# Kernel optimization log

Hardware: AMD Instinct MI355X
Metric: run time of the kernel (lower is better)

The kernel has to match this reference:

```python
import jax, jax.numpy as jnp
import numpy as np

N = 8192
D = 256
LN_EPS = 1e-5
NORM_EPS = 1e-12


def _layernorm(h, gamma, beta):
    mu = jnp.mean(h, axis=-1, keepdims=True)
    var = jnp.var(h, axis=-1, keepdims=True)
    return (h - mu) * jax.lax.rsqrt(var + LN_EPS) * gamma + beta


def _elu(z):
    return jnp.where(z > 0, z, jnp.expm1(z))


def setup_inputs() -> dict:
    key = jax.random.key(0)
    ks = jax.random.split(key, 5)
    s = 1.0 / np.sqrt(D)  # torch Linear default-ish init scale
    h = jax.random.normal(ks[0], (N, D), dtype=jnp.float32)
    x = jax.random.normal(ks[1], (N, D), dtype=jnp.float32)
    Wk = jax.random.normal(ks[2], (D, D), dtype=jnp.float32) * s
    Wq = jax.random.normal(ks[3], (D, D), dtype=jnp.float32) * s
    Wv = jax.random.normal(ks[4], (D, D), dtype=jnp.float32) * s
    ln_gamma = jnp.ones((D,), dtype=jnp.float32)
    ln_beta = jnp.zeros((D,), dtype=jnp.float32)
    semantic_weight = -1.0
    mixing = jnp.array([[semantic_weight, semantic_weight], [0.0, 0.0]], dtype=jnp.float32)
    return {"h": h, "x": x, "Wk": Wk, "Wq": Wq, "Wv": Wv,
            "ln_gamma": ln_gamma, "ln_beta": ln_beta, "mixing": mixing}


def reference(h, x, Wk, Wq, Wv, ln_gamma, ln_beta, mixing):
    h0, x0 = h, x
    hn = _layernorm(h, ln_gamma, ln_beta)                      # [N, D]
    k = hn @ Wk                                                # [N, H]
    q = hn @ Wq                                                # [N, H]
    # semantic attention: softmax over rows of k q^T / sqrt(H)
    a_h = jax.nn.softmax((k @ q.T) * (D ** -0.5), axis=-1)     # [N, N]
    # structural attention: row-L2-normalized gram matrix of x
    g = x @ x.T                                                # [N, N]
    gnorm = jnp.linalg.norm(g, axis=-1, keepdims=True)
    a_x = g / jnp.maximum(gnorm, NORM_EPS)
    # learned 2x2 mixing, softmax over dim 0 (stack @ mixing.softmax(0))
    m = jax.nn.softmax(mixing, axis=0)
    a_h_mix = a_h * m[0, 0] + a_x * m[1, 0]
    a_x_mix = a_h * m[0, 1] + a_x * m[1, 1]
    h_new = _elu((a_h_mix @ hn) @ Wv)                          # [N, D]
    x_new = a_x_mix @ x                                        # [N, D]
    h_new = h_new + h0
    x_new = x_new + x0
    return (h_new, x_new)
```

## Files before the change

kernel.cpp:

```cpp
#include <hip/hip_runtime.h>

#define N 8192
#define D 256

typedef unsigned short u16;
typedef unsigned int u32;
typedef short bf16x8 __attribute__((ext_vector_type(8)));
typedef float f32x4 __attribute__((ext_vector_type(4)));

__device__ __forceinline__ u16 f2bf(float f) {
    u32 u = __float_as_uint(f);
    u += 0x7FFFu + ((u >> 16) & 1u);
    return (u16)(u >> 16);
}
__device__ __forceinline__ float bf2f(u16 v) {
    return __uint_as_float(((u32)v) << 16);
}

#define MFMA(a, b, c) __builtin_amdgcn_mfma_f32_16x16x32_bf16((a), (b), (c), 0, 0, 0)

__global__ __launch_bounds__(256) void k_prep_ln(const float* __restrict__ h,
    const float* __restrict__ x, const float* __restrict__ gamma,
    const float* __restrict__ beta, u16* __restrict__ hnb, u16* __restrict__ xb)
{
    int lane = threadIdx.x & 63;
    int row = blockIdx.x * 4 + (threadIdx.x >> 6);
    const float4 hv = ((const float4*)(h + (size_t)row * D))[lane];
    float s = hv.x + hv.y + hv.z + hv.w;
    float s2 = hv.x * hv.x + hv.y * hv.y + hv.z * hv.z + hv.w * hv.w;
#pragma unroll
    for (int m = 1; m < 64; m <<= 1) { s += __shfl_xor(s, m); s2 += __shfl_xor(s2, m); }
    float mu = s * (1.0f / D);
    float var = s2 * (1.0f / D) - mu * mu;
    float rstd = rsqrtf(var + 1e-5f);
    const float4 gv = ((const float4*)gamma)[lane];
    const float4 bv = ((const float4*)beta)[lane];
    ushort4 o;
    o.x = f2bf((hv.x - mu) * rstd * gv.x + bv.x);
    o.y = f2bf((hv.y - mu) * rstd * gv.y + bv.y);
    o.z = f2bf((hv.z - mu) * rstd * gv.z + bv.z);
    o.w = f2bf((hv.w - mu) * rstd * gv.w + bv.w);
    ((ushort4*)(hnb + (size_t)row * D))[lane] = o;
    const float4 xv = ((const float4*)(x + (size_t)row * D))[lane];
    ushort4 xo;
    xo.x = f2bf(xv.x); xo.y = f2bf(xv.y); xo.z = f2bf(xv.z); xo.w = f2bf(xv.w);
    ((ushort4*)(xb + (size_t)row * D))[lane] = xo;
}

__global__ void k_wT(const float* __restrict__ Wk, const float* __restrict__ Wq,
                     const float* __restrict__ Wv, u16* __restrict__ wkT,
                     u16* __restrict__ wqT, u16* __restrict__ wvT)
{
    const float* src = blockIdx.y == 0 ? Wk : (blockIdx.y == 1 ? Wq : Wv);
    u16* dst = blockIdx.y == 0 ? wkT : (blockIdx.y == 1 ? wqT : wvT);
    int c = blockIdx.x, r = threadIdx.x;
    dst[c * D + r] = f2bf(src[r * D + c]);
}

__global__ __launch_bounds__(256) void k_transpose(const u16* __restrict__ s0,
    u16* __restrict__ d0, const u16* __restrict__ s1, u16* __restrict__ d1)
{
    const u16* src = blockIdx.y ? s1 : s0;
    u16* dst = blockIdx.y ? d1 : d0;
    int jb = (blockIdx.x & 127) * 64;
    int cb = (blockIdx.x >> 7) * 64;
    __shared__ u16 tile[64][72];
    int t = threadIdx.x;
#pragma unroll
    for (int i = 0; i < 2; ++i) {
        int id = t + i * 256;
        int r = id >> 3, ch = id & 7;
        uint4 v = *(const uint4*)(src + (size_t)(jb + r) * D + cb + ch * 8);
        *(uint4*)(&tile[r][ch * 8]) = v;
    }
    __syncthreads();
#pragma unroll
    for (int i = 0; i < 2; ++i) {
        int id = t + i * 256;
        int c = id >> 3, rch = id & 7;
        u16 vals[8] __attribute__((aligned(16)));
#pragma unroll
        for (int e = 0; e < 8; ++e) vals[e] = tile[rch * 8 + e][c];
        *(uint4*)(dst + (size_t)(cb + c) * N + jb + rch * 8) = *(const uint4*)vals;
    }
}

__global__ __launch_bounds__(256, 4) void k_proj_kq(const u16* __restrict__ A,
    const u16* __restrict__ wkT, const u16* __restrict__ wqT,
    u16* __restrict__ kb, u16* __restrict__ qb)
{
    int w = threadIdx.x >> 6;
    int lane = threadIdx.x & 63;
    int l16 = lane & 15, lhi = lane >> 4;
    int rows = blockIdx.x * 16;
    const u16* BT = (w >> 1) ? wqT : wkT;
    u16* out = (w >> 1) ? qb : kb;
    int colbase = (w & 1) * 128;
    const f32x4 z4 = {0.f, 0.f, 0.f, 0.f};
    f32x4 acc[8] = {z4, z4, z4, z4, z4, z4, z4, z4};
#pragma unroll
    for (int ks = 0; ks < 8; ++ks) {
        bf16x8 a = *(const bf16x8*)(A + (size_t)(rows + l16) * D + ks * 32 + lhi * 8);
#pragma unroll
        for (int cf = 0; cf < 8; ++cf) {
            bf16x8 b = *(const bf16x8*)(BT + (size_t)(colbase + cf * 16 + l16) * D + ks * 32 + lhi * 8);
            acc[cf] = MFMA(a, b, acc[cf]);
        }
    }
#pragma unroll
    for (int cf = 0; cf < 8; ++cf)
#pragma unroll
        for (int jj = 0; jj < 4; ++jj)
            out[(size_t)(rows + lhi * 4 + jj) * D + colbase + cf * 16 + l16] = f2bf(acc[cf][jj]);
}

__global__ __launch_bounds__(256) void k_small_nt(const u16* __restrict__ hnT,
    const u16* __restrict__ xT, float* __restrict__ part)
{
    const u16* P = blockIdx.y ? hnT : xT;
    const u16* Q = xT;
    int w = threadIdx.x >> 6;
    int lane = threadIdx.x & 63;
    int l16 = lane & 15, lhi = lane >> 4;
    int arow = blockIdx.x * 16;
    int bcol = w * 64;
    int n0b = blockIdx.z * 1024;
    const f32x4 z4 = {0.f, 0.f, 0.f, 0.f};
    f32x4 acc[4] = {z4, z4, z4, z4};
    for (int n0 = n0b; n0 < n0b + 1024; n0 += 32) {
        bf16x8 a = *(const bf16x8*)(P + (size_t)(arow + l16) * N + n0 + lhi * 8);
#pragma unroll
        for (int cf = 0; cf < 4; ++cf) {
            bf16x8 b = *(const bf16x8*)(Q + (size_t)(bcol + cf * 16 + l16) * N + n0 + lhi * 8);
            acc[cf] = MFMA(a, b, acc[cf]);
        }
    }
    float* dst = part + ((size_t)blockIdx.z * 2 + blockIdx.y) * 65536;
#pragma unroll
    for (int cf = 0; cf < 4; ++cf)
#pragma unroll
        for (int jj = 0; jj < 4; ++jj)
            dst[(size_t)(arow + lhi * 4 + jj) * D + bcol + cf * 16 + l16] = acc[cf][jj];
}

__global__ __launch_bounds__(256) void k_cast(const float* __restrict__ part,
    u16* __restrict__ Mb, u16* __restrict__ XHT)
{
    int t = blockIdx.x * 256 + threadIdx.x;
    int side = t >> 16, idx = t & 65535;
    float s = 0.f;
#pragma unroll
    for (int ks = 0; ks < 8; ++ks) s += part[((size_t)ks * 2 + side) * 65536 + idx];
    (side ? XHT : Mb)[idx] = f2bf(s);
}

template <int EPI>
__global__ __launch_bounds__(256, 4) void k_gemm16(const u16* __restrict__ A,
    const u16* __restrict__ BT, u16* __restrict__ outb,
    const float* __restrict__ res, float* __restrict__ outf)
{
    int w = threadIdx.x >> 6;
    int lane = threadIdx.x & 63;
    int l16 = lane & 15, lhi = lane >> 4;
    int rows = blockIdx.x * 16;
    int cols = w * 64;
    const f32x4 z4 = {0.f, 0.f, 0.f, 0.f};
    f32x4 acc[4] = {z4, z4, z4, z4};
#pragma unroll
    for (int ks = 0; ks < 8; ++ks) {
        bf16x8 a = *(const bf16x8*)(A + (size_t)(rows + l16) * D + ks * 32 + lhi * 8);
#pragma unroll
        for (int cf = 0; cf < 4; ++cf) {
            bf16x8 b = *(const bf16x8*)(BT + (size_t)(cols + cf * 16 + l16) * D + ks * 32 + lhi * 8);
            acc[cf] = MFMA(a, b, acc[cf]);
        }
    }
#pragma unroll
    for (int cf = 0; cf < 4; ++cf)
#pragma unroll
        for (int jj = 0; jj < 4; ++jj) {
            int r = rows + lhi * 4 + jj;
            int c = cols + cf * 16 + l16;
            float v = acc[cf][jj];
            if (EPI == 0) {
                outb[(size_t)r * D + c] = f2bf(v);
            } else {
                float z = v > 0.f ? v : expm1f(v);
                outf[(size_t)r * D + c] = z + res[(size_t)r * D + c];
            }
        }
}

__global__ __launch_bounds__(512, 4) void k_fused(const u16* __restrict__ kb,
    const u16* __restrict__ qb, const u16* __restrict__ hnT,
    const u16* __restrict__ xT, u16* __restrict__ accP, float* __restrict__ lpart)
{
    __shared__ u16 AK[64 * 256];
    __shared__ u16 P[64 * 256];
    const int tid = threadIdx.x;
    const int w = tid >> 6;
    const int lane = tid & 63;
    const int l16 = lane & 15, lhi = lane >> 4;
    const int wgid = blockIdx.x;
    const int xcd = wgid & 7;
    const int js = xcd >> 1;
    const int rb = ((wgid >> 3) << 1) | (xcd & 1);
    const int R0 = rb * 64;
    const int jbase = js * 2048;

    {
        int r = tid >> 3, sb = (tid & 7) * 4;
        const u16* src = kb + (size_t)(R0 + r) * D + sb * 8;
#pragma unroll
        for (int i = 0; i < 4; ++i) {
            bf16x8 v = *(const bf16x8*)(src + i * 8);
            int slotp = ((sb + i) + 4 * r) & 31;
            *(bf16x8*)(AK + r * 256 + slotp * 8) = v;
        }
    }
    __syncthreads();

    const int rg = w & 1;
    const int jf = w >> 1;
    const int t2 = w >> 2;
    const int ch = w & 3;
    const u16* T = t2 ? xT : hnT;
    const u16* Tb0 = T + (size_t)(ch * 64 + 0 * 16 + l16) * N + lhi * 8;
    const u16* Tb1 = T + (size_t)(ch * 64 + 1 * 16 + l16) * N + lhi * 8;
    const u16* Tb2 = T + (size_t)(ch * 64 + 2 * 16 + l16) * N + lhi * 8;
    const u16* Tb3 = T + (size_t)(ch * 64 + 3 * 16 + l16) * N + lhi * 8;

    const f32x4 z4 = {0.f, 0.f, 0.f, 0.f};
    f32x4 acc[16];
#pragma unroll
    for (int i = 0; i < 16; ++i) acc[i] = z4;
    f32x4 red2[2] = {z4, z4};
    bf16x8 tp0[4], tp1[4];

    for (int it = 0; it < 8; ++it) {
        const int jb = jbase + it * 256;
        asm volatile("s_waitcnt lgkmcnt(0)\n\ts_barrier" ::: "memory");

#pragma unroll
        for (int s = 0; s < 2; ++s) {
            const int jc = jb + s * 128 + jf * 32;
            f32x4 cs00 = z4, cs01 = z4, cs10 = z4, cs11 = z4;
#pragma unroll
            for (int ks = 0; ks < 8; ++ks) {
                int r0 = rg * 32 + l16;
                int r1 = rg * 32 + 16 + l16;
                int sl0 = ((ks * 4 + lhi) + 4 * r0) & 31;
                int sl1 = ((ks * 4 + lhi) + 4 * r1) & 31;
                bf16x8 a0 = *(const bf16x8*)(AK + r0 * 256 + sl0 * 8);
                bf16x8 a1 = *(const bf16x8*)(AK + r1 * 256 + sl1 * 8);
                const u16* Bq = qb + (size_t)(jc + l16) * D + ks * 32 + lhi * 8;
                bf16x8 b0 = *(const bf16x8*)(Bq);
                bf16x8 b1 = *(const bf16x8*)(Bq + 16 * D);
                cs00 = MFMA(a0, b0, cs00);
                cs01 = MFMA(a0, b1, cs01);
                cs10 = MFMA(a1, b0, cs10);
                cs11 = MFMA(a1, b1, cs11);
            }
#pragma unroll
            for (int rf = 0; rf < 2; ++rf)
#pragma unroll
                for (int cfr = 0; cfr < 2; ++cfr) {
                    f32x4 s4 = rf ? (cfr ? cs11 : cs10) : (cfr ? cs01 : cs00);
#pragma unroll
                    for (int jj = 0; jj < 4; ++jj) {
                        int row = rg * 32 + rf * 16 + lhi * 4 + jj;
                        int col = s * 128 + jf * 32 + cfr * 16 + l16;
                        float pv = __expf(s4[jj] * 0.0625f);
                        red2[rf][jj] += pv;
                        int slot = (col >> 3) ^ (row & 15);
                        *(u16*)((char*)P + row * 512 + slot * 16 + (col & 7) * 2) = f2bf(pv);
                    }
                }
        }
        tp0[0] = *(const bf16x8*)(Tb0 + jb); tp0[1] = *(const bf16x8*)(Tb1 + jb);
        tp0[2] = *(const bf16x8*)(Tb2 + jb); tp0[3] = *(const bf16x8*)(Tb3 + jb);
        tp1[0] = *(const bf16x8*)(Tb0 + jb + 32); tp1[1] = *(const bf16x8*)(Tb1 + jb + 32);
        tp1[2] = *(const bf16x8*)(Tb2 + jb + 32); tp1[3] = *(const bf16x8*)(Tb3 + jb + 32);
        asm volatile("s_waitcnt lgkmcnt(0)\n\ts_barrier" ::: "memory");

        __builtin_amdgcn_s_setprio(1);
        const char* Pb = (const char*)P;
#define PV_STEP(KF, TP)                                                             \
        {                                                                           \
            bf16x8 pa0 = *(const bf16x8*)(Pb + (0 * 16 + l16) * 512 + ((((KF) * 4 + lhi) ^ l16) << 4)); \
            bf16x8 pa1 = *(const bf16x8*)(Pb + (1 * 16 + l16) * 512 + ((((KF) * 4 + lhi) ^ l16) << 4)); \
            bf16x8 pa2 = *(const bf16x8*)(Pb + (2 * 16 + l16) * 512 + ((((KF) * 4 + lhi) ^ l16) << 4)); \
            bf16x8 pa3 = *(const bf16x8*)(Pb + (3 * 16 + l16) * 512 + ((((KF) * 4 + lhi) ^ l16) << 4)); \
            acc[0]  = MFMA(pa0, TP[0], acc[0]);  acc[1]  = MFMA(pa0, TP[1], acc[1]);  \
            acc[2]  = MFMA(pa0, TP[2], acc[2]);  acc[3]  = MFMA(pa0, TP[3], acc[3]);  \
            acc[4]  = MFMA(pa1, TP[0], acc[4]);  acc[5]  = MFMA(pa1, TP[1], acc[5]);  \
            acc[6]  = MFMA(pa1, TP[2], acc[6]);  acc[7]  = MFMA(pa1, TP[3], acc[7]);  \
            acc[8]  = MFMA(pa2, TP[0], acc[8]);  acc[9]  = MFMA(pa2, TP[1], acc[9]);  \
            acc[10] = MFMA(pa2, TP[2], acc[10]); acc[11] = MFMA(pa2, TP[3], acc[11]); \
            acc[12] = MFMA(pa3, TP[0], acc[12]); acc[13] = MFMA(pa3, TP[1], acc[13]); \
            acc[14] = MFMA(pa3, TP[2], acc[14]); acc[15] = MFMA(pa3, TP[3], acc[15]); \
            if ((KF) + 2 < 8) {                                                     \
                TP[0] = *(const bf16x8*)(Tb0 + jb + ((KF) + 2) * 32);               \
                TP[1] = *(const bf16x8*)(Tb1 + jb + ((KF) + 2) * 32);               \
                TP[2] = *(const bf16x8*)(Tb2 + jb + ((KF) + 2) * 32);               \
                TP[3] = *(const bf16x8*)(Tb3 + jb + ((KF) + 2) * 32);               \
            }                                                                       \
        }
        PV_STEP(0, tp0)
        PV_STEP(1, tp1)
        PV_STEP(2, tp0)
        PV_STEP(3, tp1)
        PV_STEP(4, tp0)
        PV_STEP(5, tp1)
        PV_STEP(6, tp0)
        PV_STEP(7, tp1)
#undef PV_STEP
        __builtin_amdgcn_s_setprio(0);
    }

    {
        u16* base = accP + ((((size_t)js * 128 + rb) * 8 + w) * 64) * 64 + lane;
#pragma unroll
        for (int rf = 0; rf < 4; ++rf)
#pragma unroll
            for (int cf = 0; cf < 4; ++cf)
#pragma unroll
                for (int jj = 0; jj < 4; ++jj) {
                    int v = (rf * 4 + cf) * 4 + jj;
                    __builtin_nontemporal_store(f2bf(acc[rf * 4 + cf][jj]), base + (size_t)v * 64);
                }
    }
#pragma unroll
    for (int rf = 0; rf < 2; ++rf)
#pragma unroll
        for (int m = 1; m < 16; m <<= 1) {
            red2[rf][0] += __shfl_xor(red2[rf][0], m);
            red2[rf][1] += __shfl_xor(red2[rf][1], m);
            red2[rf][2] += __shfl_xor(red2[rf][2], m);
            red2[rf][3] += __shfl_xor(red2[rf][3], m);
        }
    if (l16 == 0)
#pragma unroll
        for (int rf = 0; rf < 2; ++rf)
#pragma unroll
            for (int jj = 0; jj < 4; ++jj)
                atomicAdd(lpart + R0 + rg * 32 + rf * 16 + lhi * 4 + jj, red2[rf][jj]);
}

__global__ __launch_bounds__(256) void k_stats(const float* __restrict__ lpart,
    const u16* __restrict__ Ux, const u16* __restrict__ xb,
    const float* __restrict__ mixing, float* __restrict__ stats)
{
    int lane = threadIdx.x & 63;
    int row = blockIdx.x * 4 + (threadIdx.x >> 6);
    float sg = 0.f;
    {
        ushort4 yv = ((const ushort4*)(Ux + (size_t)row * D))[lane];
        ushort4 xv = ((const ushort4*)(xb + (size_t)row * D))[lane];
        sg += bf2f(yv.x) * bf2f(xv.x);
        sg += bf2f(yv.y) * bf2f(xv.y);
        sg += bf2f(yv.z) * bf2f(xv.z);
        sg += bf2f(yv.w) * bf2f(xv.w);
    }
#pragma unroll
    for (int m = 1; m < 64; m <<= 1) sg += __shfl_xor(sg, m);
    if (lane == 0) {
        float inv_l = 1.0f / lpart[row];
        float inv_g = 1.0f / fmaxf(sqrtf(fmaxf(sg, 0.f)), 1e-12f);
        float e00 = __expf(mixing[0]), e10 = __expf(mixing[2]);
        float c00 = e00 / (e00 + e10), c10 = e10 / (e00 + e10);
        float e01 = __expf(mixing[1]), e11 = __expf(mixing[3]);
        float c01 = e01 / (e01 + e11), c11 = e11 / (e01 + e11);
        float4 stv = { c00 * inv_l, c10 * inv_g, c01 * inv_l, c11 * inv_g };
        ((float4*)stats)[row] = stv;
    }
}

__global__ __launch_bounds__(256) void k_combine(const u16* __restrict__ accP,
    const float* __restrict__ stats, const u16* __restrict__ Uh,
    const u16* __restrict__ Ux, const float* __restrict__ x0,
    u16* __restrict__ hmixb, float* __restrict__ outx)
{
    int t = blockIdx.x * 256 + threadIdx.x;
    int r = t >> 7;
    int q = t & 127;
    int rb = r >> 6, rr = r & 63;
    int t2 = q >> 6;
    int cc = (q & 63) * 4;
    int wv = t2 * 4 + (cc >> 6);
    int rf = rr >> 4, lhi = (rr >> 2) & 3, jj = rr & 3;
    int cf = (cc >> 4) & 3, l16 = cc & 15;
    int v = (rf * 4 + cf) * 4 + jj;
    int lane = lhi * 16 + l16;
    float v0 = 0.f, v1 = 0.f, v2 = 0.f, v3 = 0.f;
#pragma unroll
    for (int s = 0; s < 4; ++s) {
        const u16* bp = accP + ((((size_t)s * 128 + rb) * 8 + wv) * 64 + v) * 64 + lane;
        ushort4 a = *(const ushort4*)bp;
        v0 += bf2f(a.x); v1 += bf2f(a.y); v2 += bf2f(a.z); v3 += bf2f(a.w);
    }
    float4 st = ((const float4*)stats)[r];
    if (t2 == 0) {
        int c = cc;
        ushort4 u = *(const ushort4*)(Uh + (size_t)r * D + c);
        ushort4 o;
        o.x = f2bf(st.x * v0 + st.y * bf2f(u.x));
        o.y = f2bf(st.x * v1 + st.y * bf2f(u.y));
        o.z = f2bf(st.x * v2 + st.y * bf2f(u.z));
        o.w = f2bf(st.x * v3 + st.y * bf2f(u.w));
        *(ushort4*)(hmixb + (size_t)r * D + c) = o;
    } else {
        int c = cc;
        ushort4 u = *(const ushort4*)(Ux + (size_t)r * D + c);
        float4 xv = *(const float4*)(x0 + (size_t)r * D + c);
        float4 o;
        o.x = st.z * v0 + st.w * bf2f(u.x) + xv.x;
        o.y = st.z * v1 + st.w * bf2f(u.y) + xv.y;
        o.z = st.z * v2 + st.w * bf2f(u.z) + xv.z;
        o.w = st.z * v3 + st.w * bf2f(u.w) + xv.w;
        *(float4*)(outx + (size_t)r * D + c) = o;
    }
}

extern "C" void kernel_launch(void* const* d_in, const int* in_sizes, int n_in,
                              void* d_out, int out_size, void* d_ws, size_t ws_size,
                              hipStream_t stream)
{
    const float* h = (const float*)d_in[0];
    const float* x = (const float*)d_in[1];
    const float* Wk = (const float*)d_in[2];
    const float* Wq = (const float*)d_in[3];
    const float* Wv = (const float*)d_in[4];
    const float* gamma = (const float*)d_in[5];
    const float* beta = (const float*)d_in[6];
    const float* mixing = (const float*)d_in[7];

    char* p = (char*)d_ws;
    const size_t ND2 = (size_t)N * D * 2;
    u16* hnb = (u16*)p; p += ND2;
    u16* xb = (u16*)p; p += ND2;
    u16* kb = (u16*)p; p += ND2;
    u16* qb = (u16*)p; p += ND2;
    u16* hnT = (u16*)p; p += ND2;
    u16* xT = (u16*)p; p += ND2;
    u16* Ux = (u16*)p; p += ND2;
    u16* wkT = (u16*)p; p += (size_t)D * D * 2;
    u16* wqT = (u16*)p; p += (size_t)D * D * 2;
    u16* wvT = (u16*)p; p += (size_t)D * D * 2;
    u16* Mb = (u16*)p; p += (size_t)D * D * 2;
    u16* XHT = (u16*)p; p += (size_t)D * D * 2;
    u16* accP = (u16*)p; p += (size_t)4 * N * 512 * 2;
    float* ntpart = (float*)accP;
    float* lpart = (float*)p; p += (size_t)N * 4;
    float* stats = (float*)p; p += (size_t)N * 4 * 4;
    u16* Uh = hnb;
    u16* hmixb = kb;

    float* outh = (float*)d_out;
    float* outx = outh + (size_t)N * D;

    hipMemsetAsync(lpart, 0, (size_t)N * 4, stream);
    k_prep_ln<<<N / 4, 256, 0, stream>>>(h, x, gamma, beta, hnb, xb);
    k_wT<<<dim3(256, 3), 256, 0, stream>>>(Wk, Wq, Wv, wkT, wqT, wvT);
    k_transpose<<<dim3(512, 2), 256, 0, stream>>>(hnb, hnT, xb, xT);
    k_proj_kq<<<512, 256, 0, stream>>>(hnb, wkT, wqT, kb, qb);
    k_small_nt<<<dim3(16, 2, 8), 256, 0, stream>>>(hnT, xT, ntpart);
    k_cast<<<512, 256, 0, stream>>>(ntpart, Mb, XHT);
    k_gemm16<0><<<512, 256, 0, stream>>>(xb, Mb, Ux, nullptr, nullptr);
    k_gemm16<0><<<512, 256, 0, stream>>>(xb, XHT, Uh, nullptr, nullptr);
    k_fused<<<512, 512, 0, stream>>>(kb, qb, hnT, xT, accP, lpart);
    k_stats<<<N / 4, 256, 0, stream>>>(lpart, Ux, xb, mixing, stats);
    k_combine<<<(N * 512) / 1024, 256, 0, stream>>>(accP, stats, Uh, Ux, x, hmixb, outx);
    k_gemm16<1><<<512, 256, 0, stream>>>(hmixb, wvT, nullptr, h, outh);
}
```

Before: 391.9 us.

## Remap QK^T score tiling per wave and prefetch next Q fragments into registers

The score phase now gives each wave all 64 rows and a 32-column strip, processed as two 16-column subtiles, in place of a 2x4 row/column split. Each Q B-fragment is loaded once and reused across four row fragments. The first subtile's Q fragments for the next iteration are prefetched into registers during the PV phase, hiding their global-load latency. The AK LDS swizzle changes to a simpler rotation. This raises register pressure (qpre, bq, red4) and adds more LDS A-fragment reads per wave, which could lower occupancy.

```diff
diff --git a/kernel.cpp b/kernel.cpp
--- a/kernel.cpp
+++ b/kernel.cpp
@@ -214,14 +214,12 @@
 #pragma unroll
         for (int i = 0; i < 4; ++i) {
             bf16x8 v = *(const bf16x8*)(src + i * 8);
-            int slotp = ((sb + i) + 4 * r) & 31;
+            int slotp = (sb + i + r) & 31;
             *(bf16x8*)(AK + r * 256 + slotp * 8) = v;
         }
     }
-    __syncthreads();
-
-    const int rg = w & 1;
-    const int jf = w >> 1;
+
+    const int jf = w;
     const int t2 = w >> 2;
     const int ch = w & 3;
     const u16* T = t2 ? xT : hnT;
@@ -234,47 +232,51 @@
     f32x4 acc[16];
 #pragma unroll
     for (int i = 0; i < 16; ++i) acc[i] = z4;
-    f32x4 red2[2] = {z4, z4};
-    bf16x8 tp0[4], tp1[4];
+    f32x4 red4[4] = {z4, z4, z4, z4};
+    bf16x8 tp0[4], tp1[4], qpre[8];
+
+    __syncthreads();
+
+#pragma unroll
+    for (int ks = 0; ks < 8; ++ks)
+        qpre[ks] = *(const bf16x8*)(qb + (size_t)(jbase + jf * 32 + l16) * D + ks * 32 + lhi * 8);
 
     for (int it = 0; it < 8; ++it) {
         const int jb = jbase + it * 256;
         asm volatile("s_waitcnt lgkmcnt(0)\n\ts_barrier" ::: "memory");
 
 #pragma unroll
-        for (int s = 0; s < 2; ++s) {
-            const int jc = jb + s * 128 + jf * 32;
-            f32x4 cs00 = z4, cs01 = z4, cs10 = z4, cs11 = z4;
-#pragma unroll
-            for (int ks = 0; ks < 8; ++ks) {
-                int r0 = rg * 32 + l16;
-                int r1 = rg * 32 + 16 + l16;
-                int sl0 = ((ks * 4 + lhi) + 4 * r0) & 31;
-                int sl1 = ((ks * 4 + lhi) + 4 * r1) & 31;
-                bf16x8 a0 = *(const bf16x8*)(AK + r0 * 256 + sl0 * 8);
-                bf16x8 a1 = *(const bf16x8*)(AK + r1 * 256 + sl1 * 8);
-                const u16* Bq = qb + (size_t)(jc + l16) * D + ks * 32 + lhi * 8;
-                bf16x8 b0 = *(const bf16x8*)(Bq);
-                bf16x8 b1 = *(const bf16x8*)(Bq + 16 * D);
-                cs00 = MFMA(a0, b0, cs00);
-                cs01 = MFMA(a0, b1, cs01);
-                cs10 = MFMA(a1, b0, cs10);
-                cs11 = MFMA(a1, b1, cs11);
+        for (int sub = 0; sub < 2; ++sub) {
+            const int jc = jb + jf * 32 + sub * 16;
+            f32x4 cs[4] = {z4, z4, z4, z4};
+            bf16x8 bq[8];
+            if (sub == 0) {
+#pragma unroll
+                for (int ks = 0; ks < 8; ++ks) bq[ks] = qpre[ks];
+            } else {
+#pragma unroll
+                for (int ks = 0; ks < 8; ++ks)
+                    bq[ks] = *(const bf16x8*)(qb + (size_t)(jc + l16) * D + ks * 32 + lhi * 8);
             }
 #pragma unroll
-            for (int rf = 0; rf < 2; ++rf)
-#pragma unroll
-                for (int cfr = 0; cfr < 2; ++cfr) {
-                    f32x4 s4 = rf ? (cfr ? cs11 : cs10) : (cfr ? cs01 : cs00);
-#pragma unroll
-                    for (int jj = 0; jj < 4; ++jj) {
-                        int row = rg * 32 + rf * 16 + lhi * 4 + jj;
-                        int col = s * 128 + jf * 32 + cfr * 16 + l16;
-                        float pv = __expf(s4[jj] * 0.0625f);
-                        red2[rf][jj] += pv;
-                        int slot = (col >> 3) ^ (row & 15);
-                        *(u16*)((char*)P + row * 512 + slot * 16 + (col & 7) * 2) = f2bf(pv);
-                    }
+            for (int ks = 0; ks < 8; ++ks)
+#pragma unroll
+                for (int rf = 0; rf < 4; ++rf) {
+                    int r = rf * 16 + l16;
+                    int slotp = (ks * 4 + lhi + r) & 31;
+                    bf16x8 a = *(const bf16x8*)(AK + r * 256 + slotp * 8);
+                    cs[rf] = MFMA(a, bq[ks], cs[rf]);
+                }
+#pragma unroll
+            for (int rf = 0; rf < 4; ++rf)
+#pragma unroll
+                for (int jj = 0; jj < 4; ++jj) {
+                    int row = rf * 16 + lhi * 4 + jj;
+                    int col = jf * 32 + sub * 16 + l16;
+                    float pv = __expf(cs[rf][jj] * 0.0625f);
+                    red4[rf][jj] += pv;
+                    int slot = (col >> 3) ^ (row & 15);
+                    *(u16*)((char*)P + row * 512 + slot * 16 + (col & 7) * 2) = f2bf(pv);
                 }
         }
         tp0[0] = *(const bf16x8*)(Tb0 + jb); tp0[1] = *(const bf16x8*)(Tb1 + jb);
@@ -282,6 +284,13 @@
         tp1[0] = *(const bf16x8*)(Tb0 + jb + 32); tp1[1] = *(const bf16x8*)(Tb1 + jb + 32);
         tp1[2] = *(const bf16x8*)(Tb2 + jb + 32); tp1[3] = *(const bf16x8*)(Tb3 + jb + 32);
         asm volatile("s_waitcnt lgkmcnt(0)\n\ts_barrier" ::: "memory");
+
+        {
+            const int jn = jbase + ((it + 1) & 7) * 256 + jf * 32;
+#pragma unroll
+            for (int ks = 0; ks < 8; ++ks)
+                qpre[ks] = *(const bf16x8*)(qb + (size_t)(jn + l16) * D + ks * 32 + lhi * 8);
+        }
 
         __builtin_amdgcn_s_setprio(1);
         const char* Pb = (const char*)P;
@@ -331,20 +340,20 @@
                 }
     }
 #pragma unroll
-    for (int rf = 0; rf < 2; ++rf)
+    for (int rf = 0; rf < 4; ++rf)
 #pragma unroll
         for (int m = 1; m < 16; m <<= 1) {
-            red2[rf][0] += __shfl_xor(red2[rf][0], m);
-            red2[rf][1] += __shfl_xor(red2[rf][1], m);
-            red2[rf][2] += __shfl_xor(red2[rf][2], m);
-            red2[rf][3] += __shfl_xor(red2[rf][3], m);
+            red4[rf][0] += __shfl_xor(red4[rf][0], m);
+            red4[rf][1] += __shfl_xor(red4[rf][1], m);
+            red4[rf][2] += __shfl_xor(red4[rf][2], m);
+            red4[rf][3] += __shfl_xor(red4[rf][3], m);
         }
     if (l16 == 0)
 #pragma unroll
-        for (int rf = 0; rf < 2; ++rf)
+        for (int rf = 0; rf < 4; ++rf)
 #pragma unroll
             for (int jj = 0; jj < 4; ++jj)
-                atomicAdd(lpart + R0 + rg * 32 + rf * 16 + lhi * 4 + jj, red2[rf][jj]);
+                atomicAdd(lpart + R0 + rf * 16 + lhi * 4 + jj, red4[rf][jj]);
 }
 
 __global__ __launch_bounds__(256) void k_stats(const float* __restrict__ lpart,
```

Result: slower. 494.1 us (+26.1%).
